# Kernel optimization log

Hardware: AMD Instinct MI355X
Metric: run time of the kernel (lower is better)

Reference implementation:

```python
import jax, jax.numpy as jnp
import numpy as np

B, N = 16, 4096
NPOINT, RADIUS, NSAMPLE = 1024, 0.2, 64
IN_CH = 9
MLP = [64, 64, 128]
EPS = 1e-5  # torch BatchNorm2d default eps


def setup_inputs() -> dict:
    key = jax.random.key(0)
    ks = jax.random.split(key, 2 + 4 * len(MLP))
    inp = {
        'xyz': jax.random.uniform(ks[0], (B, N, 3), jnp.float32),
        'points': jax.random.normal(ks[1], (B, N, 6), jnp.float32),
    }
    last = IN_CH
    for i, oc in enumerate(MLP):
        k = 2 + 4 * i
        inp[f'w{i}'] = jax.random.normal(ks[k], (oc, last), jnp.float32) * (1.0 / np.sqrt(last))
        inp[f'b{i}'] = jnp.zeros((oc,), jnp.float32)
        inp[f'g{i}'] = jnp.ones((oc,), jnp.float32)
        inp[f'be{i}'] = jnp.zeros((oc,), jnp.float32)
        last = oc
    return inp


def _gather(feat, idx):
    # feat [B, N, C], idx [B, ...] int -> [B, ..., C]
    return jax.vmap(lambda f, i: f[i])(feat, idx)


def _fps(xyz, npoint):
    # furthest point sampling, CUDA-kernel semantics: start at index 0.
    b, n, _ = xyz.shape

    def step(carry, _):
        dist, far = carry  # dist [B,N], far [B]
        centroid = _gather(xyz, far)  # [B,3]
        d = jnp.sum((xyz - centroid[:, None, :]) ** 2, axis=-1)  # [B,N]
        dist = jnp.minimum(dist, d)
        return (dist, jnp.argmax(dist, axis=1).astype(jnp.int32)), far

    init = (jnp.full((b, n), 1e10, xyz.dtype), jnp.zeros((b,), jnp.int32))
    _, idx = jax.lax.scan(step, init, None, length=npoint)
    return idx.T  # [B, npoint]


def _ball_query(radius, nsample, xyz, new_xyz):
    # idx [B, S, nsample]; first-found padding like the CUDA kernel.
    n = xyz.shape[1]
    # squared distances via gemm to avoid a [B,S,N,3] broadcast temp
    sqr = (jnp.sum(new_xyz ** 2, -1)[:, :, None]
           + jnp.sum(xyz ** 2, -1)[:, None, :]
           - 2.0 * jnp.einsum('bsc,bnc->bsn', new_xyz, xyz))  # [B,S,N]
    gidx = jnp.where(sqr > radius * radius, n, jnp.arange(n, dtype=jnp.int32)[None, None, :])
    gidx = jnp.sort(gidx, axis=-1)[:, :, :nsample]
    first = gidx[:, :, :1]  # centers are sampled points -> always valid
    return jnp.where(gidx == n, first, gidx)


def _forward(xyz, points, params):
    fps_idx = jax.lax.stop_gradient(_fps(xyz, NPOINT))
    new_xyz = _gather(xyz, fps_idx)  # [B,S,3]
    idx = _ball_query(RADIUS, NSAMPLE, xyz, new_xyz)  # [B,S,K]
    grouped_xyz = _gather(xyz, idx) - new_xyz[:, :, None, :]  # [B,S,K,3]
    grouped_pts = _gather(points, idx)  # [B,S,K,D]
    x = jnp.concatenate([grouped_xyz, grouped_pts], axis=-1)  # [B,S,K,C]
    for w, b, g, be in params:
        x = jnp.einsum('bskc,oc->bsko', x, w) + b  # 1x1 conv
        m = jnp.mean(x, axis=(0, 1, 2))
        v = jnp.var(x, axis=(0, 1, 2))  # biased var, as torch BN training mode
        x = jax.nn.relu(g * (x - m) * jax.lax.rsqrt(v + EPS) + be)
    new_points = jnp.max(x, axis=2).transpose(0, 2, 1)  # [B, C_out, S]
    return new_xyz, new_points


def reference(xyz, points, w0, b0, g0, be0, w1, b1, g1, be1, w2, b2, g2, be2):
    params = [(w0, b0, g0, be0), (w1, b1, g1, be1), (w2, b2, g2, be2)]
    return _forward(xyz, points, params)
```

## Files before the change

kernel.cpp:

```cpp
#include <hip/hip_runtime.h>
#include <hip/hip_bf16.h>
#include <stdint.h>

#define NBATCH 16
#define NPTS   4096
#define NPT    1024
#define NSMP   64
#define R2     0.04f
#define ICH    9
#define OC1    64
#define OC2    64
#define OC3    128
#define NROWS  (NBATCH*NPT*NSMP)
#define NBLK1  (NROWS/256)
#define NBLK23 (NROWS/128)
#define NTOTF  1048576.0f

typedef __attribute__((ext_vector_type(8))) short short8;
typedef __attribute__((ext_vector_type(4))) float f32x4;

__device__ __forceinline__ short f2bf(float f) {
    __hip_bfloat16 h = __float2bfloat16(f);
    return *reinterpret_cast<short*>(&h);
}

#define DPP64_MAX(k, CTRL, RM) do {                                          \
    unsigned _lo = (unsigned)(k); unsigned _hi = (unsigned)((k) >> 32);      \
    unsigned _nlo = (unsigned)__builtin_amdgcn_update_dpp((int)_lo, (int)_lo,\
                                                    CTRL, RM, 0xF, false);   \
    unsigned _nhi = (unsigned)__builtin_amdgcn_update_dpp((int)_hi, (int)_hi,\
                                                    CTRL, RM, 0xF, false);   \
    unsigned long long _nk = ((unsigned long long)_nhi << 32) | _nlo;        \
    if (_nk > (k)) (k) = _nk;                                                \
} while (0)

__global__ __launch_bounds__(512) void k_fps(const float* __restrict__ xyz,
                                             float* __restrict__ newxyz)
{
    const int b   = blockIdx.x;
    const int tid = threadIdx.x;
    const float* X = xyz + (size_t)b * NPTS * 3;

    __shared__ float sx[NPTS], sy[NPTS], sz[NPTS];
    __shared__ float scf[NPT * 3];
    __shared__ unsigned long long sKey[2][8];

    float px[8], py[8], pz[8], dd[8];
    unsigned comp[8];
#pragma unroll
    for (int j = 0; j < 8; ++j) {
        int p = tid + j * 512;
        px[j] = X[p*3+0]; py[j] = X[p*3+1]; pz[j] = X[p*3+2];
        sx[p] = px[j]; sy[p] = py[j]; sz[p] = pz[j];
        dd[j] = 1e10f;
        comp[j] = 0xFFFFFFFFu - (unsigned)p;
    }
    __syncthreads();

    float cx = sx[0], cy = sy[0], cz = sz[0];

    for (int it = 0; it < NPT; ++it) {
        if (tid == 0) {
            scf[it*3+0] = cx; scf[it*3+1] = cy; scf[it*3+2] = cz;
        }
        unsigned long long best = 0ull;
#pragma unroll
        for (int j = 0; j < 8; ++j) {
            float dx = px[j]-cx, dy = py[j]-cy, dz = pz[j]-cz;
            float d  = dx*dx + dy*dy + dz*dz;
            float nd = fminf(dd[j], d);
            dd[j] = nd;
            unsigned long long k =
                ((unsigned long long)__float_as_uint(nd) << 32) | comp[j];
            if (k > best) best = k;
        }
        DPP64_MAX(best, 0x111, 0xF);
        DPP64_MAX(best, 0x112, 0xF);
        DPP64_MAX(best, 0x114, 0xF);
        DPP64_MAX(best, 0x118, 0xF);
        DPP64_MAX(best, 0x142, 0xA);
        DPP64_MAX(best, 0x143, 0xC);

        const int buf = it & 1;
        if ((tid & 63) == 63) sKey[buf][tid >> 6] = best;
        __syncthreads();
        unsigned long long bb = sKey[buf][0];
#pragma unroll
        for (int w = 1; w < 8; ++w) {
            unsigned long long o = sKey[buf][w];
            bb = (o > bb) ? o : bb;
        }
        int far = (int)(0xFFFFFFFFu - (unsigned)(bb & 0xFFFFFFFFull));
        cx = sx[far]; cy = sy[far]; cz = sz[far];
    }

    __syncthreads();
    float* outb = newxyz + (size_t)b * NPT * 3;
    for (int i = tid; i < NPT*3; i += 512) outb[i] = scf[i];
}

__global__ __launch_bounds__(256) void k_ballq(const float* __restrict__ xyz,
                                               const float* __restrict__ pts,
                                               const float* __restrict__ newxyz,
                                               float* __restrict__ x0)
{
    const int wave = threadIdx.x >> 6;
    const int lane = threadIdx.x & 63;
    const int g = blockIdx.x * 4 + wave;
    const int b = g >> 10;
    const float* X = xyz + (size_t)b * NPTS * 3;
    const float* P = pts + (size_t)b * NPTS * 6;
    const float cx = newxyz[(size_t)g*3+0];
    const float cy = newxyz[(size_t)g*3+1];
    const float cz = newxyz[(size_t)g*3+2];
    const float sn = cx*cx + cy*cy + cz*cz;

    __shared__ int sFirst[4];
    int total = 0;
    for (int chunk = 0; chunk < NPTS/64; ++chunk) {
        int p = chunk*64 + lane;
        float x = X[p*3+0], y = X[p*3+1], z = X[p*3+2];
        float sp  = x*x + y*y + z*z;
        float dot = cx*x + cy*y + cz*z;
        float sqr = (sn + sp) - 2.0f*dot;
        bool inb = !(sqr > R2);
        unsigned long long mask = __ballot(inb);
        int before = __popcll(mask & ((1ull << lane) - 1ull));
        int pos = total + before;
        if (inb && pos < NSMP) {
            if (pos == 0) sFirst[wave] = p;
            float* row = x0 + ((size_t)g * NSMP + pos) * ICH;
            row[0] = x - cx; row[1] = y - cy; row[2] = z - cz;
#pragma unroll
            for (int c = 0; c < 6; ++c) row[3+c] = P[(size_t)p*6 + c];
        }
        total += (int)__popcll(mask);
        if (total >= NSMP) break;
    }
    if (total < NSMP) {
        int first = sFirst[wave];
        float x = X[first*3+0], y = X[first*3+1], z = X[first*3+2];
        float r0 = x - cx, r1 = y - cy, r2 = z - cz;
        float q0 = P[(size_t)first*6+0], q1 = P[(size_t)first*6+1], q2 = P[(size_t)first*6+2];
        float q3 = P[(size_t)first*6+3], q4 = P[(size_t)first*6+4], q5 = P[(size_t)first*6+5];
        for (int slot = total + lane; slot < NSMP; slot += 64) {
            float* row = x0 + ((size_t)g * NSMP + slot) * ICH;
            row[0]=r0; row[1]=r1; row[2]=r2;
            row[3]=q0; row[4]=q1; row[5]=q2; row[6]=q3; row[7]=q4; row[8]=q5;
        }
    }
}

__global__ __launch_bounds__(256) void k_prep(const float* __restrict__ w1,
                                              const float* __restrict__ w2,
                                              short* __restrict__ w1f,
                                              short* __restrict__ w2f)
{
    int t = blockIdx.x * 256 + threadIdx.x;
    if (t < 8*64) {
        int f = t >> 6, l = t & 63;
        int n = f >> 1, kb = f & 1;
        int col = n*16 + (l & 15);
        int k0  = kb*32 + (l >> 4)*8;
#pragma unroll
        for (int j = 0; j < 8; ++j)
            w1f[((size_t)t)*8 + j] = f2bf(w1[col*64 + k0 + j]);
    } else if (t < 8*64 + 16*64) {
        int t2 = t - 8*64;
        int f = t2 >> 6, l = t2 & 63;
        int n = f >> 1, kb = f & 1;
        int col = n*16 + (l & 15);
        int k0  = kb*32 + (l >> 4)*8;
#pragma unroll
        for (int j = 0; j < 8; ++j)
            w2f[((size_t)t2)*8 + j] = f2bf(w2[col*64 + k0 + j]);
    }
}

__global__ __launch_bounds__(256) void k_mlp1(
    const float* __restrict__ x0,
    const float* __restrict__ w0, const float* __restrict__ b0,
    float* __restrict__ pSum, float* __restrict__ pSq)
{
    __shared__ float staged[32 * 256];
    const int tid = threadIdx.x;
    const int bid = blockIdx.x;
    const size_t row = (size_t)bid * 256 + tid;

    float x[ICH];
    const float* xr = x0 + row * ICH;
#pragma unroll
    for (int c = 0; c < ICH; ++c) x[c] = xr[c];

    float h1[OC1];
#pragma unroll
    for (int o = 0; o < OC1; ++o) {
        float a = b0[o];
#pragma unroll
        for (int c = 0; c < ICH; ++c) a += w0[o*ICH + c] * x[c];
        h1[o] = a;
    }
#pragma unroll
    for (int cb = 0; cb < OC1; cb += 32) {
        __syncthreads();
#pragma unroll
        for (int o = 0; o < 32; ++o) staged[o*256 + tid] = h1[cb + o];
        __syncthreads();
        const int ch = tid >> 3, seg = tid & 7;
        const float* col = staged + ch*256 + seg*32;
        float s1 = 0.f, s2 = 0.f;
#pragma unroll
        for (int i = 0; i < 32; ++i) {
            float vv = col[(i + tid) & 31];
            s1 += vv; s2 += vv*vv;
        }
#pragma unroll
        for (int m = 1; m < 8; m <<= 1) {
            s1 += __shfl_xor(s1, m, 64);
            s2 += __shfl_xor(s2, m, 64);
        }
        if (seg == 0) {
            pSum[(size_t)bid*OC1 + cb + ch] = s1;
            pSq [(size_t)bid*OC1 + cb + ch] = s2;
        }
    }
}

template<int DEPTH>
__global__ __launch_bounds__(256) void k_mlp23(
    const float* __restrict__ x0,
    const float* __restrict__ w0, const float* __restrict__ b0,
    const short* __restrict__ w1f, const float* __restrict__ b1,
    const short* __restrict__ w2f, const float* __restrict__ b2,
    const float* __restrict__ AC,
    float* __restrict__ pSum, float* __restrict__ pSq,
    float* __restrict__ maxk)
{
    __shared__ __align__(16) short h1s[128*64];
    __shared__ __align__(16) short h2s[128*64];
    __shared__ __align__(16) short w1s[8*64*8];
    __shared__ __align__(16) short w2s[16*64*8];
    __shared__ float sS[4][128];
    __shared__ float sQ[4][128];
    __shared__ float sM[4][128];

    const int tid = threadIdx.x;
    const int bid = blockIdx.x;

    {
        const uint4* s1 = (const uint4*)w1f;
        uint4* d1 = (uint4*)w1s;
        for (int i = tid; i < 512; i += 256) d1[i] = s1[i];
        if (DEPTH == 3) {
            const uint4* s2 = (const uint4*)w2f;
            uint4* d2 = (uint4*)w2s;
            for (int i = tid; i < 1024; i += 256) d2[i] = s2[i];
        }
    }

    {
        const int rloc = tid & 127;
        const int half = __builtin_amdgcn_readfirstlane(tid >> 7);
        const size_t rowg = (size_t)bid * 128 + rloc;
        const float* xr = x0 + rowg * ICH;
        float x[ICH];
#pragma unroll
        for (int c = 0; c < ICH; ++c) x[c] = xr[c];
        const float* w0h = w0 + half*32*ICH;
        const float* b0h = b0 + half*32;
        const float* Ah  = AC + half*32;
        const float* Ch  = AC + 64 + half*32;
        float h[32];
#pragma unroll
        for (int o = 0; o < 32; ++o) {
            float a = b0h[o];
#pragma unroll
            for (int c = 0; c < ICH; ++c) a += w0h[o*ICH + c] * x[c];
            h[o] = fmaxf(Ah[o]*a + Ch[o], 0.0f);
        }
#pragma unroll
        for (int q = 0; q < 4; ++q) {
            short8 v;
#pragma unroll
            for (int j = 0; j < 8; ++j) v[j] = f2bf(h[q*8 + j]);
            int byte = (rloc*128 + half*64 + q*16) ^ ((rloc & 7) << 4);
            *(short8*)((char*)h1s + byte) = v;
        }
    }
    __syncthreads();

    const int wv = tid >> 6;
    const int l  = tid & 63;
    const int lr = l & 15, lk = l >> 4;

    f32x4 acc2[2][4];
    const f32x4 fz = {0.f, 0.f, 0.f, 0.f};
#pragma unroll
    for (int m = 0; m < 2; ++m)
#pragma unroll
        for (int n = 0; n < 4; ++n) acc2[m][n] = fz;

    short8 afr[2][2];
#pragma unroll
    for (int m = 0; m < 2; ++m)
#pragma unroll
        for (int kb = 0; kb < 2; ++kb) {
            int row = wv*32 + m*16 + lr;
            int byte = (row*128 + (kb*4 + lk)*16) ^ ((row & 7) << 4);
            afr[m][kb] = *(short8*)((char*)h1s + byte);
        }
#pragma unroll
    for (int n = 0; n < 4; ++n) {
        short8 bf0 = *(short8*)(w1s + ((n*2+0)*64 + l)*8);
        short8 bf1 = *(short8*)(w1s + ((n*2+1)*64 + l)*8);
#pragma unroll
        for (int m = 0; m < 2; ++m) {
            acc2[m][n] = __builtin_amdgcn_mfma_f32_16x16x32_bf16(afr[m][0], bf0, acc2[m][n], 0, 0, 0);
            acc2[m][n] = __builtin_amdgcn_mfma_f32_16x16x32_bf16(afr[m][1], bf1, acc2[m][n], 0, 0, 0);
        }
    }
#pragma unroll
    for (int n = 0; n < 4; ++n) {
        float bb = b1[n*16 + lr];
#pragma unroll
        for (int m = 0; m < 2; ++m)
#pragma unroll
            for (int r = 0; r < 4; ++r) acc2[m][n][r] += bb;
    }

    if (DEPTH == 2) {
#pragma unroll
        for (int n = 0; n < 4; ++n) {
            float s1 = 0.f, s2 = 0.f;
#pragma unroll
            for (int m = 0; m < 2; ++m)
#pragma unroll
                for (int r = 0; r < 4; ++r) {
                    float v = acc2[m][n][r];
                    s1 += v; s2 += v*v;
                }
            s1 += __shfl_xor(s1, 16, 64); s1 += __shfl_xor(s1, 32, 64);
            s2 += __shfl_xor(s2, 16, 64); s2 += __shfl_xor(s2, 32, 64);
            if (l < 16) { sS[wv][n*16 + l] = s1; sQ[wv][n*16 + l] = s2; }
        }
        __syncthreads();
        if (tid < OC2) {
            float a = 0.f, q = 0.f;
#pragma unroll
            for (int w = 0; w < 4; ++w) { a += sS[w][tid]; q += sQ[w][tid]; }
            pSum[(size_t)bid*OC2 + tid] = a;
            pSq [(size_t)bid*OC2 + tid] = q;
        }
        return;
    }

#pragma unroll
    for (int n = 0; n < 4; ++n) {
        int c = n*16 + lr;
        float A2 = AC[128 + c], C2 = AC[192 + c];
#pragma unroll
        for (int m = 0; m < 2; ++m)
#pragma unroll
            for (int r = 0; r < 4; ++r) {
                float v = fmaxf(A2*acc2[m][n][r] + C2, 0.0f);
                int row = wv*32 + m*16 + lk*4 + r;
                int byte = (row*128 + c*2) ^ ((row & 7) << 4);
                *(short*)((char*)h2s + byte) = f2bf(v);
            }
    }
    __syncthreads();

    f32x4 acc3[2][8];
#pragma unroll
    for (int m = 0; m < 2; ++m)
#pragma unroll
        for (int n = 0; n < 8; ++n) acc3[m][n] = fz;

    short8 afr2[2][2];
#pragma unroll
    for (int m = 0; m < 2; ++m)
#pragma unroll
        for (int kb = 0; kb < 2; ++kb) {
            int row = wv*32 + m*16 + lr;
            int byte = (row*128 + (kb*4 + lk)*16) ^ ((row & 7) << 4);
            afr2[m][kb] = *(short8*)((char*)h2s + byte);
        }
#pragma unroll
    for (int n = 0; n < 8; ++n) {
        short8 bf0 = *(short8*)(w2s + ((n*2+0)*64 + l)*8);
        short8 bf1 = *(short8*)(w2s + ((n*2+1)*64 + l)*8);
#pragma unroll
        for (int m = 0; m < 2; ++m) {
            acc3[m][n] = __builtin_amdgcn_mfma_f32_16x16x32_bf16(afr2[m][0], bf0, acc3[m][n], 0, 0, 0);
            acc3[m][n] = __builtin_amdgcn_mfma_f32_16x16x32_bf16(afr2[m][1], bf1, acc3[m][n], 0, 0, 0);
        }
    }

#pragma unroll
    for (int n = 0; n < 8; ++n) {
        float bb = b2[n*16 + lr];
        float s1 = 0.f, s2 = 0.f, mx = -3.0e38f;
#pragma unroll
        for (int m = 0; m < 2; ++m)
#pragma unroll
            for (int r = 0; r < 4; ++r) {
                float v = acc3[m][n][r] + bb;
                s1 += v; s2 += v*v; mx = fmaxf(mx, v);
            }
        s1 += __shfl_xor(s1, 16, 64); s1 += __shfl_xor(s1, 32, 64);
        s2 += __shfl_xor(s2, 16, 64); s2 += __shfl_xor(s2, 32, 64);
        mx = fmaxf(mx, __shfl_xor(mx, 16, 64));
        mx = fmaxf(mx, __shfl_xor(mx, 32, 64));
        if (l < 16) {
            sS[wv][n*16 + l] = s1;
            sQ[wv][n*16 + l] = s2;
            sM[wv][n*16 + l] = mx;
        }
    }
    __syncthreads();
    if (tid < OC3) {
        float a = 0.f, q = 0.f;
#pragma unroll
        for (int w = 0; w < 4; ++w) { a += sS[w][tid]; q += sQ[w][tid]; }
        pSum[(size_t)bid*OC3 + tid] = a;
        pSq [(size_t)bid*OC3 + tid] = q;
    }
    {
        int g = tid >> 7, c = tid & 127;
        maxk[((size_t)bid*2 + g)*OC3 + c] = fmaxf(sM[2*g][c], sM[2*g+1][c]);
    }
}

__global__ __launch_bounds__(256) void k_finalize(
    const float* __restrict__ pSum, const float* __restrict__ pSq,
    const float* __restrict__ g, const float* __restrict__ be,
    float* __restrict__ A, float* __restrict__ C, int OC, int nblk)
{
    const int o = blockIdx.x, tid = threadIdx.x;
    float s1 = 0.f, s2 = 0.f;
    for (int i = tid; i < nblk; i += 256) {
        s1 += pSum[(size_t)i*OC + o];
        s2 += pSq [(size_t)i*OC + o];
    }
    __shared__ float r1[256], r2[256];
    r1[tid] = s1; r2[tid] = s2;
    __syncthreads();
    for (int s = 128; s > 0; s >>= 1) {
        if (tid < s) { r1[tid] += r1[tid+s]; r2[tid] += r2[tid+s]; }
        __syncthreads();
    }
    if (tid == 0) {
        float mean = r1[0] * (1.0f / NTOTF);
        float var  = r2[0] * (1.0f / NTOTF) - mean*mean;
        float a = g[o] / sqrtf(var + 1e-5f);
        A[o] = a;
        C[o] = be[o] - mean * a;
    }
}

__global__ __launch_bounds__(256) void k_out(const float* __restrict__ maxk,
                                             const float* __restrict__ A,
                                             const float* __restrict__ C,
                                             float* __restrict__ out1)
{
    int idx = blockIdx.x * 256 + threadIdx.x;
    int s  = idx & (NPT - 1);
    int ch = (idx >> 10) & (OC3 - 1);
    int b  = idx >> 17;
    float v = maxk[((size_t)(b * NPT + s)) * OC3 + ch];
    out1[idx] = fmaxf(A[ch] * v + C[ch], 0.0f);
}

extern "C" void kernel_launch(void* const* d_in, const int* in_sizes, int n_in,
                              void* d_out, int out_size, void* d_ws, size_t ws_size,
                              hipStream_t stream)
{
    const float* xyz = (const float*)d_in[0];
    const float* pts = (const float*)d_in[1];
    const float* w0  = (const float*)d_in[2];
    const float* b0  = (const float*)d_in[3];
    const float* g0  = (const float*)d_in[4];
    const float* be0 = (const float*)d_in[5];
    const float* w1  = (const float*)d_in[6];
    const float* b1  = (const float*)d_in[7];
    const float* g1  = (const float*)d_in[8];
    const float* be1 = (const float*)d_in[9];
    const float* w2  = (const float*)d_in[10];
    const float* b2  = (const float*)d_in[11];
    const float* g2  = (const float*)d_in[12];
    const float* be2 = (const float*)d_in[13];

    float* out0 = (float*)d_out;
    float* out1 = out0 + (size_t)NBATCH*NPT*3;

    float* ws   = (float*)d_ws;
    float* x0   = ws;
    float* pSum = x0   + (size_t)NROWS*ICH;
    float* pSq  = pSum + (size_t)NBLK23*OC3;
    float* AC   = pSq  + (size_t)NBLK23*OC3;
    float* maxk = AC + 512;
    short* w1f  = (short*)(maxk + (size_t)NBATCH*NPT*OC3);
    short* w2f  = w1f + 8*64*8;

    k_prep <<<6, 256, 0, stream>>>(w1, w2, w1f, w2f);
    k_fps  <<<NBATCH, 512, 0, stream>>>(xyz, out0);
    k_ballq<<<(NBATCH*NPT)/4, 256, 0, stream>>>(xyz, pts, out0, x0);

    k_mlp1<<<NBLK1, 256, 0, stream>>>(x0, w0, b0, pSum, pSq);
    k_finalize<<<OC1, 256, 0, stream>>>(pSum, pSq, g0, be0, AC+0,   AC+64,  OC1, NBLK1);
    k_mlp23<2><<<NBLK23, 256, 0, stream>>>(x0, w0,b0, w1f,b1, w2f,b2, AC, pSum, pSq, maxk);
    k_finalize<<<OC2, 256, 0, stream>>>(pSum, pSq, g1, be1, AC+128, AC+192, OC2, NBLK23);
    k_mlp23<3><<<NBLK23, 256, 0, stream>>>(x0, w0,b0, w1f,b1, w2f,b2, AC, pSum, pSq, maxk);
    k_finalize<<<OC3, 256, 0, stream>>>(pSum, pSq, g2, be2, AC+256, AC+384, OC3, NBLK23);

    k_out<<<(NBATCH*OC3*NPT)/256, 256, 0, stream>>>(maxk, AC+256, AC+384, out1);
}
```

Measured before the change: 1.028 ms.

## Halve FPS block size, use packed float2 math and float4 centroid lookup

The furthest-point-sampling kernel drops from 512 to 256 threads per batch. Each thread now owns 16 points, held as float2 pairs so the distance and min updates can map to packed FP32 instructions. Shared xyz is stored interleaved with stride 4, so the next centroid comes from one 16-byte LDS read, and the cross-wave reduction shrinks from 8 to 4 waves. This targets the per-iteration barrier and reduction latency of a serial 1024-step loop, at the cost of more work per thread.

```diff
diff --git a/kernel.cpp b/kernel.cpp
--- a/kernel.cpp
+++ b/kernel.cpp
@@ -18,6 +18,7 @@
 
 typedef __attribute__((ext_vector_type(8))) short short8;
 typedef __attribute__((ext_vector_type(4))) float f32x4;
+typedef __attribute__((ext_vector_type(2))) float f32x2;
 
 __device__ __forceinline__ short f2bf(float f) {
     __hip_bfloat16 h = __float2bfloat16(f);
@@ -34,45 +35,56 @@
     if (_nk > (k)) (k) = _nk;                                                \
 } while (0)
 
-__global__ __launch_bounds__(512) void k_fps(const float* __restrict__ xyz,
+__global__ __launch_bounds__(256) void k_fps(const float* __restrict__ xyz,
                                              float* __restrict__ newxyz)
 {
     const int b   = blockIdx.x;
     const int tid = threadIdx.x;
     const float* X = xyz + (size_t)b * NPTS * 3;
 
-    __shared__ float sx[NPTS], sy[NPTS], sz[NPTS];
+    __shared__ __align__(16) float sxyz[NPTS * 4];
     __shared__ float scf[NPT * 3];
-    __shared__ unsigned long long sKey[2][8];
-
-    float px[8], py[8], pz[8], dd[8];
-    unsigned comp[8];
-#pragma unroll
-    for (int j = 0; j < 8; ++j) {
-        int p = tid + j * 512;
-        px[j] = X[p*3+0]; py[j] = X[p*3+1]; pz[j] = X[p*3+2];
-        sx[p] = px[j]; sy[p] = py[j]; sz[p] = pz[j];
-        dd[j] = 1e10f;
-        comp[j] = 0xFFFFFFFFu - (unsigned)p;
+    __shared__ unsigned long long sKey[2][4];
+
+    f32x2 px[8], py[8], pz[8], dd[8];
+    unsigned comp[16];
+#pragma unroll
+    for (int m = 0; m < 8; ++m) {
+        int p0 = tid + (2*m+0) * 256;
+        int p1 = tid + (2*m+1) * 256;
+        float x0 = X[p0*3+0], y0 = X[p0*3+1], z0 = X[p0*3+2];
+        float x1 = X[p1*3+0], y1 = X[p1*3+1], z1 = X[p1*3+2];
+        px[m] = (f32x2){x0, x1}; py[m] = (f32x2){y0, y1}; pz[m] = (f32x2){z0, z1};
+        sxyz[p0*4+0] = x0; sxyz[p0*4+1] = y0; sxyz[p0*4+2] = z0;
+        sxyz[p1*4+0] = x1; sxyz[p1*4+1] = y1; sxyz[p1*4+2] = z1;
+        dd[m] = (f32x2){1e10f, 1e10f};
+        comp[2*m+0] = 0xFFFFFFFFu - (unsigned)p0;
+        comp[2*m+1] = 0xFFFFFFFFu - (unsigned)p1;
     }
     __syncthreads();
 
-    float cx = sx[0], cy = sy[0], cz = sz[0];
+    float cx = sxyz[0], cy = sxyz[1], cz = sxyz[2];
 
     for (int it = 0; it < NPT; ++it) {
         if (tid == 0) {
             scf[it*3+0] = cx; scf[it*3+1] = cy; scf[it*3+2] = cz;
         }
+        const f32x2 c2x = (f32x2){cx, cx};
+        const f32x2 c2y = (f32x2){cy, cy};
+        const f32x2 c2z = (f32x2){cz, cz};
         unsigned long long best = 0ull;
 #pragma unroll
-        for (int j = 0; j < 8; ++j) {
-            float dx = px[j]-cx, dy = py[j]-cy, dz = pz[j]-cz;
-            float d  = dx*dx + dy*dy + dz*dz;
-            float nd = fminf(dd[j], d);
-            dd[j] = nd;
-            unsigned long long k =
-                ((unsigned long long)__float_as_uint(nd) << 32) | comp[j];
-            if (k > best) best = k;
+        for (int m = 0; m < 8; ++m) {
+            f32x2 dx = px[m] - c2x, dy = py[m] - c2y, dz = pz[m] - c2z;
+            f32x2 d  = dx*dx + dy*dy + dz*dz;
+            f32x2 nd = __builtin_elementwise_min(dd[m], d);
+            dd[m] = nd;
+            unsigned long long k0 =
+                ((unsigned long long)__float_as_uint(nd.x) << 32) | comp[2*m+0];
+            if (k0 > best) best = k0;
+            unsigned long long k1 =
+                ((unsigned long long)__float_as_uint(nd.y) << 32) | comp[2*m+1];
+            if (k1 > best) best = k1;
         }
         DPP64_MAX(best, 0x111, 0xF);
         DPP64_MAX(best, 0x112, 0xF);
@@ -86,17 +98,18 @@
         __syncthreads();
         unsigned long long bb = sKey[buf][0];
 #pragma unroll
-        for (int w = 1; w < 8; ++w) {
+        for (int w = 1; w < 4; ++w) {
             unsigned long long o = sKey[buf][w];
             bb = (o > bb) ? o : bb;
         }
         int far = (int)(0xFFFFFFFFu - (unsigned)(bb & 0xFFFFFFFFull));
-        cx = sx[far]; cy = sy[far]; cz = sz[far];
+        const f32x4 c4 = *(const f32x4*)&sxyz[far*4];
+        cx = c4.x; cy = c4.y; cz = c4.z;
     }
 
     __syncthreads();
     float* outb = newxyz + (size_t)b * NPT * 3;
-    for (int i = tid; i < NPT*3; i += 512) outb[i] = scf[i];
+    for (int i = tid; i < NPT*3; i += 256) outb[i] = scf[i];
 }
 
 __global__ __launch_bounds__(256) void k_ballq(const float* __restrict__ xyz,
@@ -503,7 +516,7 @@
     short* w2f  = w1f + 8*64*8;
 
     k_prep <<<6, 256, 0, stream>>>(w1, w2, w1f, w2f);
-    k_fps  <<<NBATCH, 512, 0, stream>>>(xyz, out0);
+    k_fps  <<<NBATCH, 256, 0, stream>>>(xyz, out0);
     k_ballq<<<(NBATCH*NPT)/4, 256, 0, stream>>>(xyz, pts, out0, x0);
 
     k_mlp1<<<NBLK1, 256, 0, stream>>>(x0, w0, b0, pSum, pSq);
```

Measured after the change: 931.6 us. 9.4% less time.
